# Performance work log

Measured on AMD Instinct MI355X. Metric: run time of the kernel, lower is better.

## Reference

```python
import jax, jax.numpy as jnp
import numpy as np
from jax import lax

B, CIN, H, W = 2, 64, 56, 56
CMID, COUT = 128, 128


def _pos_enc(h, w, c, dtype):
    # 2D sinusoidal encoding: first half of channels encode row, second half column.
    def enc1d(L, dim):
        pos = jnp.arange(L, dtype=jnp.float32)[:, None]
        div = jnp.exp(-jnp.log(10000.0) * jnp.arange(0, dim, 2, dtype=jnp.float32) / dim)
        ang = pos * div
        e = jnp.zeros((L, dim), jnp.float32)
        e = e.at[:, 0::2].set(jnp.sin(ang)).at[:, 1::2].set(jnp.cos(ang))
        return e
    ch = c // 2
    eh = enc1d(h, ch)            # (H, ch)
    ew = enc1d(w, c - ch)        # (W, c-ch)
    pe = jnp.concatenate([
        jnp.broadcast_to(eh[:, None, :], (h, w, ch)),
        jnp.broadcast_to(ew[None, :, :], (h, w, c - ch)),
    ], axis=-1)
    return pe.astype(dtype)


def _nbr_idx(L, k, d):
    # NATTEN-style dilated neighborhood indices with border clamping, per dilation
    # residue group. Returns (L, k) int32 indices into [0, L).
    i = jnp.arange(L)
    p, r = i // d, i % d
    Lg = (L - r - 1) // d + 1                      # group length per residue
    start = jnp.clip(p - k // 2, 0, jnp.maximum(Lg - k, 0))
    j = jnp.arange(k)
    idx = r[:, None] + (start[:, None] + j[None, :]) * d
    return jnp.minimum(idx, L - 1)


def setup_inputs() -> dict:
    key = jax.random.key(0)
    ks = jax.random.split(key, 9)
    s3 = 1.0 / np.sqrt(CIN * 9)
    s1 = 1.0 / np.sqrt(CMID)
    return {
        "x": jax.random.normal(ks[0], (B, CIN, H, W), jnp.float32),
        "conv_w": jax.random.normal(ks[1], (CMID, CIN, 3, 3), jnp.float32) * s3,
        "conv_b": jax.random.normal(ks[2], (CMID,), jnp.float32) * 0.01,
        "q_w": jax.random.normal(ks[3], (CMID, CMID), jnp.float32) * s1,
        "q_b": jax.random.normal(ks[4], (CMID,), jnp.float32) * 0.01,
        "k_w": jax.random.normal(ks[5], (CMID, CMID), jnp.float32) * s1,
        "k_b": jax.random.normal(ks[6], (CMID,), jnp.float32) * 0.01,
        "v_w": jax.random.normal(ks[7], (COUT, CMID), jnp.float32) * s1,
        "v_b": jax.random.normal(ks[8], (COUT,), jnp.float32) * 0.01,
        "kernel_size": 7,
        "dilation": 2,
    }


def reference(x, conv_w, conv_b, q_w, q_b, k_w, k_b, v_w, v_b, kernel_size, dilation):
    # shared 3x3 conv projection (SAME padding), NCHW
    sf = lax.conv_general_dilated(x, conv_w, (1, 1), 'SAME',
                                  dimension_numbers=('NCHW', 'OIHW', 'NCHW'))
    sf = sf + conv_b[None, :, None, None]
    sf = jnp.transpose(sf, (0, 2, 3, 1))                      # (B,H,W,Cmid)
    q = jnp.einsum('bhwc,oc->bhwo', sf, q_w) + q_b            # 1x1 convs
    k = jnp.einsum('bhwc,oc->bhwo', sf, k_w) + k_b
    v = jnp.einsum('bhwc,oc->bhwo', sf, v_w) + v_b            # (B,H,W,Cout)
    pe = _pos_enc(q.shape[1], q.shape[2], q.shape[3], q.dtype)
    peb = jnp.broadcast_to(pe[None], q.shape)
    q = jnp.concatenate([q, peb], axis=-1)                    # (B,H,W,2Cmid)
    k = jnp.concatenate([k, peb], axis=-1)

    kk = int(kernel_size)
    dd = int(dilation)
    ih = _nbr_idx(q.shape[1], kk, dd)                         # (H,kk)
    iw = _nbr_idx(q.shape[2], kk, dd)                         # (W,kk)
    # gather dilated neighborhoods: (B,H,W,kk,kk,D)
    knb = k[:, ih[:, None, :, None], iw[None, :, None, :], :]
    vnb = v[:, ih[:, None, :, None], iw[None, :, None, :], :]
    scale = 1.0 / jnp.sqrt(jnp.asarray(q.shape[-1], q.dtype))
    logits = jnp.einsum('bhwd,bhwuvd->bhwuv', q, knb) * scale
    Bq, Hq, Wq = logits.shape[:3]
    attn = jax.nn.softmax(logits.reshape(Bq, Hq, Wq, kk * kk), axis=-1)
    attn = attn.reshape(Bq, Hq, Wq, kk, kk)
    out = jnp.einsum('bhwuv,bhwuvd->bhwd', attn, vnb)         # (B,H,W,Cout)
    return out
```

## Files before the change

### kernel.cpp

```cpp
#include <hip/hip_runtime.h>
#include <hip/hip_bf16.h>
#include <math.h>

#define BB   2
#define HH   56
#define WW   56
#define CIN  64
#define CMID 128

typedef short bf8_t __attribute__((ext_vector_type(8)));
typedef float f4_t  __attribute__((ext_vector_type(4)));
typedef _Float16 h2_t __attribute__((ext_vector_type(2)));
typedef _Float16 h8_t __attribute__((ext_vector_type(8)));

#define QH_OFF  0
#define KH_OFF  401408
#define VH_OFF  802816
#define AS_OFF  1204224
#define WFH_OFF 1204736
#define WFL_OFF 1241600
#define W2H_OFF 1278464
#define W2L_OFF 1303040

__device__ __forceinline__ unsigned short f2bf(float f) {
    unsigned int u = __builtin_bit_cast(unsigned int, f);
    u += 0x7fffu + ((u >> 16) & 1u);
    return (unsigned short)(u >> 16);
}
__device__ __forceinline__ float bf2f(unsigned short h) {
    unsigned int u = ((unsigned int)h) << 16;
    return __builtin_bit_cast(float, u);
}

__global__ __launch_bounds__(256) void prep_w(
    const float* __restrict__ cw, const float* __restrict__ qw,
    const float* __restrict__ kw, const float* __restrict__ vw,
    unsigned short* __restrict__ wfh, unsigned short* __restrict__ wfl,
    unsigned short* __restrict__ w2h, unsigned short* __restrict__ w2l,
    float* __restrict__ As)
{
    int idx = blockIdx.x * 256 + threadIdx.x;
    if (idx < 9 * 2 * 8 * 64 * 8) {
        int j    = idx & 7;
        int lane = (idx >> 3) & 63;
        int o16  = (idx >> 9) & 7;
        int kk32 = (idx >> 12) & 1;
        int seg  = idx >> 13;
        int o = o16 * 16 + (lane & 15);
        int c = kk32 * 32 + (lane >> 4) * 8 + j;
        float wv = cw[(o * 64 + c) * 9 + seg];
        unsigned short hi = f2bf(wv);
        wfh[idx] = hi; wfl[idx] = f2bf(wv - bf2f(hi));
    }
    if (idx < 4 * 24 * 64 * 8) {
        int j    = idx & 7;
        int lane = (idx >> 3) & 63;
        int rest = idx >> 9;
        int n16  = rest % 24;
        int kk32 = rest / 24;
        int n = n16 * 16 + (lane & 15);
        int c = kk32 * 32 + (lane >> 4) * 8 + j;
        int which = n >> 7, o = n & 127;
        const float* src = which == 0 ? qw : (which == 1 ? kw : vw);
        float wv = src[o * 128 + c];
        unsigned short hi = f2bf(wv);
        w2h[idx] = hi; w2l[idx] = f2bf(wv - bf2f(hi));
    }
    if (blockIdx.x == 288) {
        for (int t = threadIdx.x; t < 56 * 7; t += 256) {
            int i = t / 7, j = t % 7;
            int p = i >> 1;
            int start = p - 3;
            if (start < 0) start = 0;
            if (start > 21) start = 21;
            int nidx = (i & 1) + (start + j) * 2;
            float delta = (float)(i - nidx);
            float acc = 0.f;
            for (int u = 0; u < 32; ++u) {
                float d = expf(-9.210340371976184f * (float)u * 0.03125f);
                acc += cosf(delta * d);
            }
            As[t] = acc * 0.0625f;
        }
    }
}

__global__ __launch_bounds__(512) void conv_qkv_mfma(
    const float* __restrict__ x,
    const unsigned short* __restrict__ wfh, const unsigned short* __restrict__ wfl,
    const float* __restrict__ cb,
    const unsigned short* __restrict__ w2h, const unsigned short* __restrict__ w2l,
    const float* __restrict__ qb, const float* __restrict__ kb,
    const float* __restrict__ vb,
    _Float16* __restrict__ qh16, _Float16* __restrict__ kh16,
    _Float16* __restrict__ vh16)
{
    __shared__ char xsb[2][3 * 34 * 64 * 2];
    __shared__ char sfb[2][32 * 128 * 2];
    const int wt = blockIdx.x;
    const int h  = blockIdx.y;
    const int b  = blockIdx.z;
    const int w0 = wt * 28;
    const int tid = threadIdx.x;

    for (int idx = tid; idx < 3 * 64 * 34; idx += 512) {
        int dh  = idx / (64 * 34);
        int rem = idx % (64 * 34);
        int c   = rem / 34;
        int row = rem % 34;
        int y   = h + dh - 1;
        int wg  = w0 - 1 + row;
        float val = 0.f;
        if ((unsigned)y < HH && (unsigned)wg < WW)
            val = x[((b * CIN + c) * HH + y) * WW + wg];
        unsigned short hi = f2bf(val);
        unsigned short lo = f2bf(val - bf2f(hi));
        int byteoff = (((dh * 34 + row) * 64 + c) * 2) ^ ((row & 7) << 4);
        *(unsigned short*)(xsb[0] + byteoff) = hi;
        *(unsigned short*)(xsb[1] + byteoff) = lo;
    }
    __syncthreads();

    const int lane   = tid & 63;
    const int wid    = tid >> 6;
    const int wm     = wid >> 2;
    const int wn     = wid & 3;
    const int lane15 = lane & 15;
    const int lanehi = lane >> 4;

    f4_t acc[2] = {};
    for (int seg = 0; seg < 9; ++seg) {
        const int dh = seg / 3, dw = seg % 3;
#pragma unroll
        for (int kk32 = 0; kk32 < 2; ++kk32) {
            int row = wm * 16 + lane15 + dw;
            int byteoff = (((dh * 34 + row) * 64 + kk32 * 32 + lanehi * 8) * 2)
                          ^ ((row & 7) << 4);
            bf8_t ah = *(const bf8_t*)(xsb[0] + byteoff);
            bf8_t al = *(const bf8_t*)(xsb[1] + byteoff);
#pragma unroll
            for (int nf = 0; nf < 2; ++nf) {
                int fidx = (((seg * 2 + kk32) * 8 + (wn * 2 + nf)) * 64 + lane) * 8;
                bf8_t bh = *(const bf8_t*)(wfh + fidx);
                bf8_t bl = *(const bf8_t*)(wfl + fidx);
                acc[nf] = __builtin_amdgcn_mfma_f32_16x16x32_bf16(ah, bh, acc[nf], 0, 0, 0);
                acc[nf] = __builtin_amdgcn_mfma_f32_16x16x32_bf16(al, bh, acc[nf], 0, 0, 0);
                acc[nf] = __builtin_amdgcn_mfma_f32_16x16x32_bf16(ah, bl, acc[nf], 0, 0, 0);
            }
        }
    }

#pragma unroll
    for (int nf = 0; nf < 2; ++nf) {
        int ch = wn * 32 + nf * 16 + lane15;
        float bias = cb[ch];
#pragma unroll
        for (int r = 0; r < 4; ++r) {
            int m = wm * 16 + lanehi * 4 + r;
            float val = acc[nf][r] + bias;
            unsigned short hi = f2bf(val);
            unsigned short lo = f2bf(val - bf2f(hi));
            int byteoff = ((m * 128 + ch) * 2) ^ ((m & 7) << 4);
            *(unsigned short*)(sfb[0] + byteoff) = hi;
            *(unsigned short*)(sfb[1] + byteoff) = lo;
        }
    }
    __syncthreads();

    f4_t acc2[6] = {};
#pragma unroll
    for (int kk32 = 0; kk32 < 4; ++kk32) {
        int row = wm * 16 + lane15;
        int byteoff = ((row * 128 + kk32 * 32 + lanehi * 8) * 2) ^ ((row & 7) << 4);
        bf8_t ah = *(const bf8_t*)(sfb[0] + byteoff);
        bf8_t al = *(const bf8_t*)(sfb[1] + byteoff);
#pragma unroll
        for (int nf = 0; nf < 6; ++nf) {
            int fidx = ((kk32 * 24 + wn * 6 + nf) * 64 + lane) * 8;
            bf8_t bh = *(const bf8_t*)(w2h + fidx);
            bf8_t bl = *(const bf8_t*)(w2l + fidx);
            acc2[nf] = __builtin_amdgcn_mfma_f32_16x16x32_bf16(ah, bh, acc2[nf], 0, 0, 0);
            acc2[nf] = __builtin_amdgcn_mfma_f32_16x16x32_bf16(al, bh, acc2[nf], 0, 0, 0);
            acc2[nf] = __builtin_amdgcn_mfma_f32_16x16x32_bf16(ah, bl, acc2[nf], 0, 0, 0);
        }
    }

#pragma unroll
    for (int nf = 0; nf < 6; ++nf) {
        int n = wn * 96 + nf * 16 + lane15;
        int which = n >> 7;
        int o = n & 127;
        const float* bp = which == 0 ? qb : (which == 1 ? kb : vb);
        float bias = bp[o];
#pragma unroll
        for (int r = 0; r < 4; ++r) {
            int m = wm * 16 + lanehi * 4 + r;
            int wpos = w0 + m;
            if (wpos < WW) {
                float val = acc2[nf][r] + bias;
                int di = ((b * HH + h) * WW + wpos) * CMID + o;
                if (which == 0)      qh16[di] = (_Float16)(val * 0.0625f);
                else if (which == 1) kh16[di] = (_Float16)val;
                else                 vh16[di] = (_Float16)val;
            }
        }
    }
}

__global__ __launch_bounds__(256) void attn_tiled(
    const _Float16* __restrict__ qh, const _Float16* __restrict__ kh,
    const _Float16* __restrict__ vh, const float* __restrict__ As,
    float* __restrict__ out)
{
    __shared__ char Kb[112 * 256];
    __shared__ char Vb[100 * 256];
    __shared__ char Qb[16 * 256];
    __shared__ float lg[16 * 113];
    __shared__ float awv[4][64];

    const int tid = threadIdx.x;
    int bid = blockIdx.x;
    const int b   = bid / 196; bid %= 196;
    const int par = bid / 49;
    const int t49 = bid % 49;
    const int rh = par >> 1, rw = par & 1;
    const int p0 = (t49 / 7) * 4, q0 = (t49 % 7) * 4;

    int smh = p0 - 3; if (smh < 0) smh = 0; if (smh > 21) smh = 21;
    int smw = q0 - 3; if (smw < 0) smw = 0; if (smw > 21) smw = 21;

    const int rlo = tid >> 4;
    const int t16 = tid & 15;

    {
        int qi = rlo;
        int pp = p0 + (qi >> 2), qq = q0 + (qi & 3);
        int hq = rh + 2 * pp, wq = rw + 2 * qq;
        const char* src = (const char*)(qh + ((b * HH + hq) * WW + wq) * CMID);
        uint4 d = *(const uint4*)(src + t16 * 16);
        *(uint4*)(Qb + qi * 256 + ((t16 * 16) ^ ((qi & 7) << 4))) = d;
    }
    for (int r0 = 0; r0 < 112; r0 += 16) {
        int n = r0 + rlo;
        int i = n / 10, jj = n % 10;
        int ihs = smh + i; if (ihs > 27) ihs = 27;
        int iws = smw + jj; if (iws > 27) iws = 27;
        int ih = rh + 2 * ihs, iw = rw + 2 * iws;
        const char* src = (const char*)(kh + ((b * HH + ih) * WW + iw) * CMID);
        uint4 d = *(const uint4*)(src + t16 * 16);
        *(uint4*)(Kb + n * 256 + ((t16 * 16) ^ ((n & 7) << 4))) = d;
    }
    for (int r0 = 0; r0 < 112; r0 += 16) {
        int n = r0 + rlo;
        if (n < 100) {
            int i = n / 10, jj = n % 10;
            int ihs = smh + i; if (ihs > 27) ihs = 27;
            int iws = smw + jj; if (iws > 27) iws = 27;
            int ih = rh + 2 * ihs, iw = rw + 2 * iws;
            const char* src = (const char*)(vh + ((b * HH + ih) * WW + iw) * CMID);
            uint4 d = *(const uint4*)(src + t16 * 16);
            *(uint4*)(Vb + n * 256 + t16 * 16) = d;
        }
    }
    __syncthreads();

    const int lane   = tid & 63;
    const int wvid   = tid >> 6;
    const int lane15 = lane & 15;
    const int lanehi = lane >> 4;

    {
        int nfs = wvid * 2;
        int nfe = nfs + 2; if (nfe > 7) nfe = 7;
        for (int nf = nfs; nf < nfe; ++nf) {
            f4_t acc = {};
            int n = nf * 16 + lane15;
#pragma unroll
            for (int kk = 0; kk < 4; ++kk) {
                int koff = kk * 64 + lanehi * 16;
                h8_t a  = *(const h8_t*)(Qb + lane15 * 256 + (koff ^ ((lane15 & 7) << 4)));
                h8_t bb = *(const h8_t*)(Kb + n * 256      + (koff ^ ((n & 7) << 4)));
                acc = __builtin_amdgcn_mfma_f32_16x16x32_f16(a, bb, acc, 0, 0, 0);
            }
#pragma unroll
            for (int r = 0; r < 4; ++r)
                lg[(lanehi * 4 + r) * 113 + n] = acc[r];
        }
    }
    __syncthreads();

    const int u   = lane / 7;
    const int vv2 = lane % 7;

    for (int t = 0; t < 4; ++t) {
        int qi = wvid * 4 + t;
        int pp = p0 + (qi >> 2), qq = q0 + (qi & 3);
        int hq = rh + 2 * pp, wq = rw + 2 * qq;
        int sp = pp - 3; if (sp < 0) sp = 0; if (sp > 21) sp = 21;
        int sq = qq - 3; if (sq < 0) sq = 0; if (sq > 21) sq = 21;
        int ru = sp - smh, rc = sq - smw;

        float logit = -INFINITY;
        if (lane < 49) {
            int n = (ru + u) * 10 + (rc + vv2);
            logit = lg[qi * 113 + n] + As[hq * 7 + u] + As[wq * 7 + vv2];
        }
        float m = logit;
#pragma unroll
        for (int s = 32; s > 0; s >>= 1)
            m = fmaxf(m, __shfl_xor(m, s, 64));
        float e = (lane < 49) ? expf(logit - m) : 0.f;
        float ssum = e;
#pragma unroll
        for (int s = 32; s > 0; s >>= 1)
            ssum += __shfl_xor(ssum, s, 64);
        awv[wvid][lane] = e / ssum;

        float o0 = 0.f, o1 = 0.f;
#pragma unroll
        for (int u2 = 0; u2 < 7; ++u2) {
            int rowb = (ru + u2) * 10 + rc;
#pragma unroll
            for (int v2 = 0; v2 < 7; ++v2) {
                float a2 = awv[wvid][u2 * 7 + v2];
                unsigned pv = *(const unsigned*)(Vb + (rowb + v2) * 256 + lane * 4);
                h2_t ph = __builtin_bit_cast(h2_t, pv);
                o0 += a2 * (float)ph[0];
                o1 += a2 * (float)ph[1];
            }
        }
        int g = (b * HH + hq) * WW + wq;
        *(float2*)(out + g * CMID + lane * 2) = make_float2(o0, o1);
    }
}

extern "C" void kernel_launch(void* const* d_in, const int* in_sizes, int n_in,
                              void* d_out, int out_size, void* d_ws, size_t ws_size,
                              hipStream_t stream)
{
    const float* x  = (const float*)d_in[0];
    const float* cw = (const float*)d_in[1];
    const float* cb = (const float*)d_in[2];
    const float* qw = (const float*)d_in[3];
    const float* qb = (const float*)d_in[4];
    const float* kw = (const float*)d_in[5];
    const float* kb = (const float*)d_in[6];
    const float* vw = (const float*)d_in[7];
    const float* vb = (const float*)d_in[8];

    float* ws = (float*)d_ws;
    _Float16* qhx = (_Float16*)(ws + QH_OFF);
    _Float16* khx = (_Float16*)(ws + KH_OFF);
    _Float16* vhx = (_Float16*)(ws + VH_OFF);
    float* As = ws + AS_OFF;
    unsigned short* wfh = (unsigned short*)(ws + WFH_OFF);
    unsigned short* wfl = (unsigned short*)(ws + WFL_OFF);
    unsigned short* w2h = (unsigned short*)(ws + W2H_OFF);
    unsigned short* w2l = (unsigned short*)(ws + W2L_OFF);
    float* out = (float*)d_out;

    hipLaunchKernelGGL(prep_w, dim3(289), dim3(256), 0, stream,
                       cw, qw, kw, vw, wfh, wfl, w2h, w2l, As);
    hipLaunchKernelGGL(conv_qkv_mfma, dim3(2, 56, 2), dim3(512), 0, stream,
                       x, wfh, wfl, cb, w2h, w2l, qb, kb, vb, qhx, khx, vhx);
    hipLaunchKernelGGL(attn_tiled, dim3(392), dim3(256), 0, stream,
                       qhx, khx, vhx, As, out);
}
```

Measured before the change: 117.1 us.

## Share one LDS buffer for K and V, load Q into registers, remap blocks

```diff
diff --git a/kernel.cpp b/kernel.cpp
--- a/kernel.cpp
+++ b/kernel.cpp
@@ -212,14 +212,13 @@
     const _Float16* __restrict__ vh, const float* __restrict__ As,
     float* __restrict__ out)
 {
-    __shared__ char Kb[112 * 256];
-    __shared__ char Vb[100 * 256];
-    __shared__ char Qb[16 * 256];
-    __shared__ float lg[16 * 113];
+    __shared__ char KVb[100 * 256];
+    __shared__ float lg[16 * 100];
     __shared__ float awv[4][64];
 
     const int tid = threadIdx.x;
-    int bid = blockIdx.x;
+    int bid0 = blockIdx.x;
+    int bid = (bid0 & 7) * 49 + (bid0 >> 3);
     const int b   = bid / 196; bid %= 196;
     const int par = bid / 49;
     const int t49 = bid % 49;
@@ -231,25 +230,59 @@
 
     const int rlo = tid >> 4;
     const int t16 = tid & 15;
-
-    {
-        int qi = rlo;
-        int pp = p0 + (qi >> 2), qq = q0 + (qi & 3);
-        int hq = rh + 2 * pp, wq = rw + 2 * qq;
-        const char* src = (const char*)(qh + ((b * HH + hq) * WW + wq) * CMID);
-        uint4 d = *(const uint4*)(src + t16 * 16);
-        *(uint4*)(Qb + qi * 256 + ((t16 * 16) ^ ((qi & 7) << 4))) = d;
-    }
+    const int lane   = tid & 63;
+    const int wvid   = tid >> 6;
+    const int lane15 = lane & 15;
+    const int lanehi = lane >> 4;
+
+    int qp  = p0 + (lane15 >> 2), qq2 = q0 + (lane15 & 3);
+    int hql = rh + 2 * qp, wql = rw + 2 * qq2;
+    const _Float16* qrow = qh + ((b * HH + hql) * WW + wql) * CMID + lanehi * 8;
+    h8_t a0 = *(const h8_t*)(qrow);
+    h8_t a1 = *(const h8_t*)(qrow + 32);
+    h8_t a2 = *(const h8_t*)(qrow + 64);
+    h8_t a3 = *(const h8_t*)(qrow + 96);
+
     for (int r0 = 0; r0 < 112; r0 += 16) {
         int n = r0 + rlo;
-        int i = n / 10, jj = n % 10;
-        int ihs = smh + i; if (ihs > 27) ihs = 27;
-        int iws = smw + jj; if (iws > 27) iws = 27;
-        int ih = rh + 2 * ihs, iw = rw + 2 * iws;
-        const char* src = (const char*)(kh + ((b * HH + ih) * WW + iw) * CMID);
-        uint4 d = *(const uint4*)(src + t16 * 16);
-        *(uint4*)(Kb + n * 256 + ((t16 * 16) ^ ((n & 7) << 4))) = d;
-    }
+        if (n < 100) {
+            int i = n / 10, jj = n % 10;
+            int ihs = smh + i; if (ihs > 27) ihs = 27;
+            int iws = smw + jj; if (iws > 27) iws = 27;
+            int ih = rh + 2 * ihs, iw = rw + 2 * iws;
+            const char* src = (const char*)(kh + ((b * HH + ih) * WW + iw) * CMID);
+            uint4 d = *(const uint4*)(src + t16 * 16);
+            *(uint4*)(KVb + n * 256 + ((t16 * 16) ^ ((n & 7) << 4))) = d;
+        }
+    }
+    __syncthreads();
+
+    {
+        int nfs = wvid * 2;
+        int nfe = nfs + 2; if (nfe > 7) nfe = 7;
+        for (int nf = nfs; nf < nfe; ++nf) {
+            f4_t acc = {};
+            int n = nf * 16 + lane15;
+            int neff = n < 100 ? n : n - 16;
+            const int swz = (neff & 7) << 4;
+            const char* kb0 = KVb + neff * 256;
+            h8_t b0 = *(const h8_t*)(kb0 + ((lanehi * 16) ^ swz));
+            h8_t b1 = *(const h8_t*)(kb0 + ((64 + lanehi * 16) ^ swz));
+            h8_t b2 = *(const h8_t*)(kb0 + ((128 + lanehi * 16) ^ swz));
+            h8_t b3 = *(const h8_t*)(kb0 + ((192 + lanehi * 16) ^ swz));
+            acc = __builtin_amdgcn_mfma_f32_16x16x32_f16(a0, b0, acc, 0, 0, 0);
+            acc = __builtin_amdgcn_mfma_f32_16x16x32_f16(a1, b1, acc, 0, 0, 0);
+            acc = __builtin_amdgcn_mfma_f32_16x16x32_f16(a2, b2, acc, 0, 0, 0);
+            acc = __builtin_amdgcn_mfma_f32_16x16x32_f16(a3, b3, acc, 0, 0, 0);
+            if (n < 100) {
+#pragma unroll
+                for (int r = 0; r < 4; ++r)
+                    lg[(lanehi * 4 + r) * 100 + n] = acc[r];
+            }
+        }
+    }
+    __syncthreads();
+
     for (int r0 = 0; r0 < 112; r0 += 16) {
         int n = r0 + rlo;
         if (n < 100) {
@@ -259,32 +292,7 @@
             int ih = rh + 2 * ihs, iw = rw + 2 * iws;
             const char* src = (const char*)(vh + ((b * HH + ih) * WW + iw) * CMID);
             uint4 d = *(const uint4*)(src + t16 * 16);
-            *(uint4*)(Vb + n * 256 + t16 * 16) = d;
-        }
-    }
-    __syncthreads();
-
-    const int lane   = tid & 63;
-    const int wvid   = tid >> 6;
-    const int lane15 = lane & 15;
-    const int lanehi = lane >> 4;
-
-    {
-        int nfs = wvid * 2;
-        int nfe = nfs + 2; if (nfe > 7) nfe = 7;
-        for (int nf = nfs; nf < nfe; ++nf) {
-            f4_t acc = {};
-            int n = nf * 16 + lane15;
-#pragma unroll
-            for (int kk = 0; kk < 4; ++kk) {
-                int koff = kk * 64 + lanehi * 16;
-                h8_t a  = *(const h8_t*)(Qb + lane15 * 256 + (koff ^ ((lane15 & 7) << 4)));
-                h8_t bb = *(const h8_t*)(Kb + n * 256      + (koff ^ ((n & 7) << 4)));
-                acc = __builtin_amdgcn_mfma_f32_16x16x32_f16(a, bb, acc, 0, 0, 0);
-            }
-#pragma unroll
-            for (int r = 0; r < 4; ++r)
-                lg[(lanehi * 4 + r) * 113 + n] = acc[r];
+            *(uint4*)(KVb + n * 256 + t16 * 16) = d;
         }
     }
     __syncthreads();
@@ -303,7 +311,7 @@
         float logit = -INFINITY;
         if (lane < 49) {
             int n = (ru + u) * 10 + (rc + vv2);
-            logit = lg[qi * 113 + n] + As[hq * 7 + u] + As[wq * 7 + vv2];
+            logit = lg[qi * 100 + n] + As[hq * 7 + u] + As[wq * 7 + vv2];
         }
         float m = logit;
 #pragma unroll
@@ -322,11 +330,11 @@
             int rowb = (ru + u2) * 10 + rc;
 #pragma unroll
             for (int v2 = 0; v2 < 7; ++v2) {
-                float a2 = awv[wvid][u2 * 7 + v2];
-                unsigned pv = *(const unsigned*)(Vb + (rowb + v2) * 256 + lane * 4);
+                float a2w = awv[wvid][u2 * 7 + v2];
+                unsigned pv = *(const unsigned*)(KVb + (rowb + v2) * 256 + lane * 4);
                 h2_t ph = __builtin_bit_cast(h2_t, pv);
-                o0 += a2 * (float)ph[0];
-                o1 += a2 * (float)ph[1];
+                o0 += a2w * (float)ph[0];
+                o1 += a2w * (float)ph[1];
             }
         }
         int g = (b * HH + hq) * WW + wq;
```

Result: no change. 117.0 us (-0.1%).
